# Optimization experiments

Measured on AMD Instinct MI355X. Metric: run time of the kernel, lower is better.

Reference implementation:

```python
import jax, jax.numpy as jnp
import numpy as np

BETA = 1.0  # nn.SmoothL1Loss() default; module's self.beta=0.5 is never used


def smooth_l1(d):
    ad = jnp.abs(d)
    return jnp.where(ad < BETA, 0.5 * d * d / BETA, ad - 0.5 * BETA)


def setup_inputs() -> dict:
    key = jax.random.key(0)
    k1, k2, k3 = jax.random.split(key, 3)
    B, T, D = 32, 2048, 512
    preds = jax.random.normal(k1, (B, T, D), dtype=jnp.float32)
    targets = jax.random.normal(k2, (B, T, D), dtype=jnp.float32)
    # lengths in [1, T], sorted descending (pack_padded_sequence convention)
    decode_lengths = jnp.sort(jax.random.randint(k3, (B,), 1, T + 1))[::-1]
    return {"preds": preds, "targets": targets, "decode_lengths": decode_lengths}


def reference(preds, targets, decode_lengths):
    B, T, D = preds.shape
    mask = (jnp.arange(T)[None, :] < decode_lengths[:, None]).astype(preds.dtype)  # [B,T]
    lens = decode_lengths.astype(preds.dtype)[:, None]  # [B,1]

    # sentence loss: SmoothL1 between per-sample time-means, mean over D, summed over B
    pred_mean = jnp.einsum('btd,bt->bd', preds, mask) / lens
    targ_mean = jnp.einsum('btd,bt->bd', targets, mask) / lens
    sentence_loss = jnp.sum(jnp.mean(smooth_l1(pred_mean - targ_mean), axis=1))

    # word loss: SmoothL1 over all valid (packed) elements, mean reduction
    elem = smooth_l1(preds - targets) * mask[:, :, None]
    n_valid = jnp.sum(decode_lengths).astype(preds.dtype) * D
    word_loss = jnp.sum(elem) / n_valid

    return word_loss + sentence_loss / B
```

## Files before the change

### kernel.cpp

```cpp
#include <hip/hip_runtime.h>


#define BATCH 32
#define TLEN  2048
#define DDIM  512
#define ROWS_PER_BLOCK 32
#define P1_THREADS 128

__device__ __forceinline__ float sl1(float d) {
    float ad = fabsf(d);
    return ad < 1.0f ? 0.5f * d * d : ad - 0.5f;
}

__global__ __launch_bounds__(P1_THREADS)
void pass1(const float* __restrict__ preds, const float* __restrict__ targs,
           const int* __restrict__ lens,
           float* __restrict__ colp, float* __restrict__ colt,
           float* __restrict__ wacc)
{
    const int b     = blockIdx.x;
    const int chunk = blockIdx.y;
    const int len   = lens[b];
    const int t0    = chunk * ROWS_PER_BLOCK;
    if (t0 >= len) return;
    const int t1 = min(t0 + ROWS_PER_BLOCK, len);

    const float4* __restrict__ p4 =
        (const float4*)(preds + (size_t)b * TLEN * DDIM);
    const float4* __restrict__ q4 =
        (const float4*)(targs + (size_t)b * TLEN * DDIM);
    const int lane4 = threadIdx.x;

    float4 sp = make_float4(0.f, 0.f, 0.f, 0.f);
    float4 st = make_float4(0.f, 0.f, 0.f, 0.f);
    float  w  = 0.f;

    for (int t = t0; t < t1; ++t) {
        float4 p = p4[(size_t)t * (DDIM / 4) + lane4];
        float4 q = q4[(size_t)t * (DDIM / 4) + lane4];
        sp.x += p.x; sp.y += p.y; sp.z += p.z; sp.w += p.w;
        st.x += q.x; st.y += q.y; st.z += q.z; st.w += q.w;
        w += sl1(p.x - q.x) + sl1(p.y - q.y) + sl1(p.z - q.z) + sl1(p.w - q.w);
    }

    float* cp = colp + b * DDIM + lane4 * 4;
    float* ct = colt + b * DDIM + lane4 * 4;
    atomicAdd(cp + 0, sp.x); atomicAdd(cp + 1, sp.y);
    atomicAdd(cp + 2, sp.z); atomicAdd(cp + 3, sp.w);
    atomicAdd(ct + 0, st.x); atomicAdd(ct + 1, st.y);
    atomicAdd(ct + 2, st.z); atomicAdd(ct + 3, st.w);

    #pragma unroll
    for (int off = 32; off; off >>= 1) w += __shfl_down(w, off);
    __shared__ float ws[P1_THREADS / 64];
    if ((threadIdx.x & 63) == 0) ws[threadIdx.x >> 6] = w;
    __syncthreads();
    if (threadIdx.x == 0) {
        float tot = 0.f;
        #pragma unroll
        for (int i = 0; i < P1_THREADS / 64; ++i) tot += ws[i];
        atomicAdd(wacc, tot);
    }
}

__global__ __launch_bounds__(1024)
void pass2(const float* __restrict__ colp, const float* __restrict__ colt,
           const int* __restrict__ lens, const float* __restrict__ wacc,
           float* __restrict__ out)
{
    const int tid = threadIdx.x;
    float s = 0.f;
    for (int i = tid; i < BATCH * DDIM; i += 1024) {
        const int b = i >> 9;
        const float L = (float)lens[b];
        const float d = (colp[i] - colt[i]) / L;
        s += sl1(d);
    }
    #pragma unroll
    for (int off = 32; off; off >>= 1) s += __shfl_down(s, off);
    __shared__ float red[16];
    if ((tid & 63) == 0) red[tid >> 6] = s;
    __syncthreads();
    if (tid == 0) {
        float sent = 0.f;
        #pragma unroll
        for (int i = 0; i < 16; ++i) sent += red[i];
        float nvalid = 0.f;
        for (int b = 0; b < BATCH; ++b) nvalid += (float)lens[b];
        const float word_loss = wacc[0] / (nvalid * (float)DDIM);
        const float sent_loss = sent / ((float)DDIM * (float)BATCH);
        out[0] = word_loss + sent_loss;
    }
}

extern "C" void kernel_launch(void* const* d_in, const int* in_sizes, int n_in,
                              void* d_out, int out_size, void* d_ws, size_t ws_size,
                              hipStream_t stream) {
    const float* preds = (const float*)d_in[0];
    const float* targs = (const float*)d_in[1];
    const int*   lens  = (const int*)d_in[2];
    float* out = (float*)d_out;

    float* colp = (float*)d_ws;
    float* colt = colp + BATCH * DDIM;
    float* wacc = colt + BATCH * DDIM;
    const size_t ws_bytes = (size_t)(2 * BATCH * DDIM + 1) * sizeof(float);
    hipMemsetAsync(d_ws, 0, ws_bytes, stream);

    dim3 grid1(BATCH, TLEN / ROWS_PER_BLOCK);
    pass1<<<grid1, P1_THREADS, 0, stream>>>(preds, targs, lens, colp, colt, wacc);
    pass2<<<1, 1024, 0, stream>>>(colp, colt, lens, wacc, out);
}
```

Baseline: 273.9 us.

## Replace global atomics with per-chunk partial sums reduced in second pass

Pass1 now writes per-(batch,chunk) column partial sums and word-loss partials to workspace with plain float4 stores instead of scalar atomicAdds. Pass2 then reduces the valid chunks per batch itself. This removes atomic contention and the workspace memset launch. In exchange, pass2 runs as a single 1024-thread block and must read up to 64 chunks per column, about 8 MB of partials, which may make it slow.

```diff
diff --git a/kernel.cpp b/kernel.cpp
--- a/kernel.cpp
+++ b/kernel.cpp
@@ -4,7 +4,8 @@
 #define BATCH 32
 #define TLEN  2048
 #define DDIM  512
-#define ROWS_PER_BLOCK 32
+#define ROWS  32
+#define NCHUNK (TLEN / ROWS)
 #define P1_THREADS 128
 
 __device__ __forceinline__ float sl1(float d) {
@@ -15,20 +16,19 @@
 __global__ __launch_bounds__(P1_THREADS)
 void pass1(const float* __restrict__ preds, const float* __restrict__ targs,
            const int* __restrict__ lens,
-           float* __restrict__ colp, float* __restrict__ colt,
-           float* __restrict__ wacc)
+           float* __restrict__ partp,
+           float* __restrict__ partt,
+           float* __restrict__ wpart)
 {
     const int b     = blockIdx.x;
     const int chunk = blockIdx.y;
     const int len   = lens[b];
-    const int t0    = chunk * ROWS_PER_BLOCK;
+    const int t0    = chunk * ROWS;
     if (t0 >= len) return;
-    const int t1 = min(t0 + ROWS_PER_BLOCK, len);
+    const int t1 = min(t0 + ROWS, len);
 
-    const float4* __restrict__ p4 =
-        (const float4*)(preds + (size_t)b * TLEN * DDIM);
-    const float4* __restrict__ q4 =
-        (const float4*)(targs + (size_t)b * TLEN * DDIM);
+    const float4* __restrict__ p4 = (const float4*)(preds + (size_t)b * TLEN * DDIM);
+    const float4* __restrict__ q4 = (const float4*)(targs + (size_t)b * TLEN * DDIM);
     const int lane4 = threadIdx.x;
 
     float4 sp = make_float4(0.f, 0.f, 0.f, 0.f);
@@ -43,53 +43,70 @@
         w += sl1(p.x - q.x) + sl1(p.y - q.y) + sl1(p.z - q.z) + sl1(p.w - q.w);
     }
 
-    float* cp = colp + b * DDIM + lane4 * 4;
-    float* ct = colt + b * DDIM + lane4 * 4;
-    atomicAdd(cp + 0, sp.x); atomicAdd(cp + 1, sp.y);
-    atomicAdd(cp + 2, sp.z); atomicAdd(cp + 3, sp.w);
-    atomicAdd(ct + 0, st.x); atomicAdd(ct + 1, st.y);
-    atomicAdd(ct + 2, st.z); atomicAdd(ct + 3, st.w);
+    float4* op = (float4*)(partp + ((size_t)b * NCHUNK + chunk) * DDIM);
+    float4* ot = (float4*)(partt + ((size_t)b * NCHUNK + chunk) * DDIM);
+    op[lane4] = sp;
+    ot[lane4] = st;
 
     #pragma unroll
     for (int off = 32; off; off >>= 1) w += __shfl_down(w, off);
     __shared__ float ws[P1_THREADS / 64];
     if ((threadIdx.x & 63) == 0) ws[threadIdx.x >> 6] = w;
     __syncthreads();
-    if (threadIdx.x == 0) {
-        float tot = 0.f;
-        #pragma unroll
-        for (int i = 0; i < P1_THREADS / 64; ++i) tot += ws[i];
-        atomicAdd(wacc, tot);
-    }
+    if (threadIdx.x == 0) wpart[b * NCHUNK + chunk] = ws[0] + ws[1];
 }
 
 __global__ __launch_bounds__(1024)
-void pass2(const float* __restrict__ colp, const float* __restrict__ colt,
-           const int* __restrict__ lens, const float* __restrict__ wacc,
+void pass2(const float* __restrict__ partp, const float* __restrict__ partt,
+           const int* __restrict__ lens, const float* __restrict__ wpart,
            float* __restrict__ out)
 {
     const int tid = threadIdx.x;
+
     float s = 0.f;
-    for (int i = tid; i < BATCH * DDIM; i += 1024) {
-        const int b = i >> 9;
-        const float L = (float)lens[b];
-        const float d = (colp[i] - colt[i]) / L;
-        s += sl1(d);
+    for (int i = tid; i < BATCH * (DDIM / 4); i += 1024) {
+        const int b   = i >> 7;
+        const int d4  = i & 127;
+        const int len = lens[b];
+        const int nch = (len + ROWS - 1) / ROWS;
+        const float4* pp = (const float4*)(partp + (size_t)b * NCHUNK * DDIM) + d4;
+        const float4* tt = (const float4*)(partt + (size_t)b * NCHUNK * DDIM) + d4;
+        float4 cp = make_float4(0.f, 0.f, 0.f, 0.f);
+        float4 ct = make_float4(0.f, 0.f, 0.f, 0.f);
+        for (int c = 0; c < nch; ++c) {
+            float4 a  = pp[(size_t)c * (DDIM / 4)];
+            float4 bb = tt[(size_t)c * (DDIM / 4)];
+            cp.x += a.x; cp.y += a.y; cp.z += a.z; cp.w += a.w;
+            ct.x += bb.x; ct.y += bb.y; ct.z += bb.z; ct.w += bb.w;
+        }
+        const float invL = 1.f / (float)len;
+        s += sl1((cp.x - ct.x) * invL) + sl1((cp.y - ct.y) * invL)
+           + sl1((cp.z - ct.z) * invL) + sl1((cp.w - ct.w) * invL);
     }
+
+    float wsum = 0.f;
+    for (int i = tid; i < BATCH * NCHUNK; i += 1024) {
+        const int b = i >> 6;
+        const int c = i & (NCHUNK - 1);
+        if (c * ROWS < lens[b]) wsum += wpart[i];
+    }
+
     #pragma unroll
-    for (int off = 32; off; off >>= 1) s += __shfl_down(s, off);
-    __shared__ float red[16];
-    if ((tid & 63) == 0) red[tid >> 6] = s;
+    for (int off = 32; off; off >>= 1) {
+        s    += __shfl_down(s, off);
+        wsum += __shfl_down(wsum, off);
+    }
+    __shared__ float rs[16], rw[16];
+    if ((tid & 63) == 0) { rs[tid >> 6] = s; rw[tid >> 6] = wsum; }
     __syncthreads();
     if (tid == 0) {
-        float sent = 0.f;
+        float sent = 0.f, word = 0.f;
         #pragma unroll
-        for (int i = 0; i < 16; ++i) sent += red[i];
+        for (int i = 0; i < 16; ++i) { sent += rs[i]; word += rw[i]; }
         float nvalid = 0.f;
         for (int b = 0; b < BATCH; ++b) nvalid += (float)lens[b];
-        const float word_loss = wacc[0] / (nvalid * (float)DDIM);
-        const float sent_loss = sent / ((float)DDIM * (float)BATCH);
-        out[0] = word_loss + sent_loss;
+        out[0] = word / (nvalid * (float)DDIM)
+               + sent / ((float)DDIM * (float)BATCH);
     }
 }
 
@@ -101,13 +118,11 @@
     const int*   lens  = (const int*)d_in[2];
     float* out = (float*)d_out;
 
-    float* colp = (float*)d_ws;
-    float* colt = colp + BATCH * DDIM;
-    float* wacc = colt + BATCH * DDIM;
-    const size_t ws_bytes = (size_t)(2 * BATCH * DDIM + 1) * sizeof(float);
-    hipMemsetAsync(d_ws, 0, ws_bytes, stream);
+    float* partp = (float*)d_ws;
+    float* partt = partp + (size_t)BATCH * NCHUNK * DDIM;
+    float* wpart = partt + (size_t)BATCH * NCHUNK * DDIM;
 
-    dim3 grid1(BATCH, TLEN / ROWS_PER_BLOCK);
-    pass1<<<grid1, P1_THREADS, 0, stream>>>(preds, targs, lens, colp, colt, wacc);
-    pass2<<<1, 1024, 0, stream>>>(colp, colt, lens, wacc, out);
+    dim3 grid1(BATCH, NCHUNK);
+    pass1<<<grid1, P1_THREADS, 0, stream>>>(preds, targs, lens, partp, partt, wpart);
+    pass2<<<1, 1024, 0, stream>>>(partp, partt, lens, wpart, out);
 }
```

Measured after the change: 291.5 us. 6.4% more time.
